# Kernel optimization log

Hardware: AMD Instinct MI355X
Metric: run time of the kernel (lower is better)

## Reference

```python
import jax, jax.numpy as jnp
import numpy as np

N, K = 50000, 16
IN_FEATS, HIDDEN, T2V = 128, 128, 64


def time2vec(t, w0, b0, W, B):
    # t: [..., 1] -> [..., T2V]; linear term + sin periodic terms
    lin = t * w0 + b0                      # [..., 1]
    per = jnp.sin(t * W + B)               # [..., T2V-1]
    return jnp.concatenate([lin, per], axis=-1)


def setup_inputs() -> dict:
    key = jax.random.key(0)
    ks = jax.random.split(key, 12)
    s = 0.05
    return {
        "x": jax.random.normal(ks[0], (N, IN_FEATS), jnp.float32),
        "ts": jax.random.uniform(ks[1], (N, K), jnp.float32),
        "idx": jax.random.randint(ks[2], (N, K), 0, N),
        "t2v_w0": jax.random.normal(ks[3], (1,), jnp.float32),
        "t2v_b0": jax.random.normal(ks[4], (1,), jnp.float32),
        "t2v_W": jax.random.normal(ks[5], (T2V - 1,), jnp.float32),
        "t2v_B": jax.random.normal(ks[6], (T2V - 1,), jnp.float32),
        "Wq": jax.random.normal(ks[7], (IN_FEATS + T2V, HIDDEN), jnp.float32) * s,
        "Wk": jax.random.normal(ks[8], (IN_FEATS + T2V, HIDDEN), jnp.float32) * s,
        "Wv": jax.random.normal(ks[9], (IN_FEATS + T2V, HIDDEN), jnp.float32) * s,
        "Wo": jax.random.normal(ks[10], (HIDDEN, HIDDEN), jnp.float32) * s,
        "bo": jnp.zeros((HIDDEN,), jnp.float32),
    }


def reference(x, ts, idx, t2v_w0, t2v_b0, t2v_W, t2v_B, Wq, Wk, Wv, Wo, bo):
    # Self representation: node feats + time2vec of zero time offset
    te_self = time2vec(jnp.zeros((x.shape[0], 1), x.dtype), t2v_w0, t2v_b0, t2v_W, t2v_B)  # [N, T2V]
    h_self = jnp.concatenate([x, te_self], axis=-1)           # [N, IN+T2V]

    # Neighbor gather + time2vec of interaction times
    x_nbr = x[idx]                                             # [N, K, IN]
    te_nbr = time2vec(ts[..., None], t2v_w0, t2v_b0, t2v_W, t2v_B)  # [N, K, T2V]
    h_nbr = jnp.concatenate([x_nbr, te_nbr], axis=-1)          # [N, K, IN+T2V]

    # Single-head scaled dot-product attention over neighbors
    q = h_self @ Wq                                            # [N, H]
    k = jnp.einsum('nkf,fh->nkh', h_nbr, Wk)                   # [N, K, H]
    v = jnp.einsum('nkf,fh->nkh', h_nbr, Wv)                   # [N, K, H]
    scores = jnp.einsum('nh,nkh->nk', q, k) / jnp.sqrt(jnp.asarray(HIDDEN, x.dtype))
    attn = jax.nn.softmax(scores, axis=-1)                     # [N, K]
    agg = jnp.einsum('nk,nkh->nh', attn, v)                    # [N, H]

    return jax.nn.relu(agg @ Wo + bo)                          # [N, H]
```

## Files before the change

### kernel.cpp

```cpp
#include <hip/hip_runtime.h>
#include <math.h>

#define NN 50000
#define SCL 0.08838834764831845f

#define QC    0
#define CQK   128
#define WT    192
#define BT    256
#define UBASE 320
#define QXB   0
#define KXB   6400000
#define VOB   12800000
#define QKXB  19200000
#define WCAT  22400000
#define WVOP  22457344

typedef __attribute__((ext_vector_type(8))) short bf16x8;
typedef __attribute__((ext_vector_type(4))) float f32x4;

__device__ __forceinline__ float bfl(unsigned int u) {
  union { unsigned int i; float f; } v; v.i = u << 16; return v.f;
}
__device__ __forceinline__ float bfh(unsigned int u) {
  union { unsigned int i; float f; } v; v.i = u & 0xffff0000u; return v.f;
}
__device__ __forceinline__ unsigned short f2bf(float f) {
  union { float f; unsigned int i; } v; v.f = f;
  return (unsigned short)((v.i + 0x7fff + ((v.i >> 16) & 1)) >> 16);
}

__global__ __launch_bounds__(128) void tgat_prep(
    const float* __restrict__ Wq, const float* __restrict__ Wk,
    const float* __restrict__ Wv, const float* __restrict__ Wo,
    const float* __restrict__ t2v_w0, const float* __restrict__ t2v_b0,
    const float* __restrict__ t2v_W, const float* __restrict__ t2v_B,
    float* __restrict__ ws, unsigned short* __restrict__ ub) {
  const int h = threadIdx.x;
  const int b = blockIdx.x;
  __shared__ float row_s[128];

  if (b < 128) {
    const float* wvrow = Wv + b * 128;
    float acc = 0.f;
#pragma unroll 8
    for (int f = 0; f < 128; ++f) acc += wvrow[f] * Wo[f * 128 + h];
    ub[WCAT + (256 + h) * 128 + b] = f2bf(acc);
  } else if (b < 192) {
    const int j = b - 128;
    const float* wvrow = Wv + (128 + j) * 128;
    float acc = 0.f;
#pragma unroll 8
    for (int f = 0; f < 128; ++f) acc += wvrow[f] * Wo[f * 128 + h];
    row_s[h] = acc;
    __syncthreads();
    if (h < 64) {
      unsigned* wp = (unsigned*)(ub + WVOP);
      wp[j * 64 + h] = (unsigned)f2bf(row_s[2 * h]) |
                       ((unsigned)f2bf(row_s[2 * h + 1]) << 16);
    }
  } else if (b == 192) {
    float acc = t2v_b0[0] * Wq[128 * 128 + h];
    for (int j = 1; j < 64; ++j)
      acc += __sinf(t2v_B[j - 1]) * Wq[(128 + j) * 128 + h];
    ws[QC + h] = acc;
  } else if (b < 321) {
    const int f = b - 193;
    if (h < 64) {
      const float* wqrow = Wq + f * 128;
      const float* wkrow = Wk + (128 + h) * 128;
      float acc = 0.f;
#pragma unroll 8
      for (int i = 0; i < 128; ++i) acc += wqrow[i] * wkrow[i];
      ub[WCAT + (384 + h) * 128 + f] = f2bf(SCL * acc);
    }
  } else if (b < 577) {
    const int c = b - 321;
    const float v = (c < 128) ? Wq[h * 128 + c] : Wk[h * 128 + (c - 128)];
    ub[WCAT + c * 128 + h] = f2bf(v);
  } else {
    if (h < 64) {
      ws[WT + h] = (h == 0) ? t2v_w0[0] : t2v_W[h - 1];
      ws[BT + h] = (h == 0) ? t2v_b0[0] : t2v_B[h - 1];
    }
  }
}

__global__ __launch_bounds__(64) void tgat_prep2(
    const float* __restrict__ Wk, float* __restrict__ ws) {
  const int j = threadIdx.x;
  const float* wkrow = Wk + (128 + j) * 128;
  float acc = 0.f;
#pragma unroll 8
  for (int i = 0; i < 128; ++i) acc += ws[QC + i] * wkrow[i];
  ws[CQK + j] = SCL * acc;
}

__global__ __launch_bounds__(256, 4) void tgat_precomp_mfma(
    const float* __restrict__ x, float* ws) {
  const int lane = threadIdx.x & 63;
  const int wv = threadIdx.x >> 6;
  const int mr = blockIdx.x * 128 + wv * 32;
  unsigned short* ub = (unsigned short*)(ws + UBASE);
  const unsigned short* wc = ub + WCAT;
  const int arow = lane & 15;
  const int ko = (lane >> 4) * 8;
  const int rbase = (lane >> 4) * 4;

  bf16x8 afr[2][4];
#pragma unroll
  for (int tile = 0; tile < 2; ++tile) {
    const int row = mr + tile * 16 + arow;
    const float* xrow = x + (size_t)((row < NN) ? row : (NN - 1)) * 128;
#pragma unroll
    for (int kk = 0; kk < 4; ++kk) {
      const float4 lo = *(const float4*)(xrow + kk * 32 + ko);
      const float4 hi = *(const float4*)(xrow + kk * 32 + ko + 4);
      bf16x8 f;
      f[0] = (short)f2bf(lo.x); f[1] = (short)f2bf(lo.y);
      f[2] = (short)f2bf(lo.z); f[3] = (short)f2bf(lo.w);
      f[4] = (short)f2bf(hi.x); f[5] = (short)f2bf(hi.y);
      f[6] = (short)f2bf(hi.z); f[7] = (short)f2bf(hi.w);
      afr[tile][kk] = f;
    }
  }

  unsigned short* qxb  = ub + QXB;
  unsigned short* kxb  = ub + KXB;
  unsigned short* vob  = ub + VOB;
  unsigned short* qkxb = ub + QKXB;

#pragma unroll 2
  for (int ct = 0; ct < 28; ++ct) {
    const int col = ct * 16 + arow;
    bf16x8 bfr[4];
#pragma unroll
    for (int kk = 0; kk < 4; ++kk)
      bfr[kk] = *(const bf16x8*)(wc + (size_t)col * 128 + kk * 32 + ko);
    f32x4 acc0 = {0.f, 0.f, 0.f, 0.f}, acc1 = {0.f, 0.f, 0.f, 0.f};
#pragma unroll
    for (int kk = 0; kk < 4; ++kk) {
      acc0 = __builtin_amdgcn_mfma_f32_16x16x32_bf16(afr[0][kk], bfr[kk], acc0, 0, 0, 0);
      acc1 = __builtin_amdgcn_mfma_f32_16x16x32_bf16(afr[1][kk], bfr[kk], acc1, 0, 0, 0);
    }

    const int gc = ct * 16 + arow;
#pragma unroll
    for (int tile = 0; tile < 2; ++tile) {
      const f32x4 acc = tile ? acc1 : acc0;
      const int r0 = mr + tile * 16 + rbase;
      if (ct < 8) {
        const float qc = ws[QC + gc];
#pragma unroll
        for (int r = 0; r < 4; ++r)
          if (r0 + r < NN)
            qxb[(size_t)(r0 + r) * 128 + gc] = f2bf((acc[r] + qc) * SCL);
      } else if (ct < 16) {
#pragma unroll
        for (int r = 0; r < 4; ++r)
          if (r0 + r < NN)
            kxb[(size_t)(r0 + r) * 128 + (gc - 128)] = f2bf(acc[r]);
      } else if (ct < 24) {
#pragma unroll
        for (int r = 0; r < 4; ++r)
          if (r0 + r < NN)
            vob[(size_t)(r0 + r) * 128 + (gc - 256)] = f2bf(acc[r]);
      } else {
        const float cq = ws[CQK + gc - 384];
#pragma unroll
        for (int r = 0; r < 4; ++r)
          if (r0 + r < NN)
            qkxb[(size_t)(r0 + r) * 64 + (gc - 384)] = f2bf(acc[r] + cq);
      }
    }
  }
}

__global__ __launch_bounds__(256, 4) void tgat_main(
    const float* __restrict__ ts, const int* __restrict__ idx,
    const float* __restrict__ bo, const float* __restrict__ ws,
    float* __restrict__ out) {
  const int lane = threadIdx.x & 63;
  const int wv   = threadIdx.x >> 6;
  const int my_k = lane >> 2, my_c = lane & 3;

  __shared__ float lds[4 * 1312];
  __shared__ unsigned wvo_l[4096];
  float* te_s = lds + wv * 1312;
  float* s_s  = te_s + 1088;
  float* q_s  = te_s + 1104;
  float* qk_s = te_s + 1248;

  const unsigned short* ubr = (const unsigned short*)(ws + UBASE);
  const unsigned short* qxb  = ubr + QXB;
  const unsigned short* kxb  = ubr + KXB;
  const unsigned short* vob  = ubr + VOB;
  const unsigned short* qkxb = ubr + QKXB;

  const int n = blockIdx.x * 4 + wv;

  {
    const uint4* wvp = (const uint4*)(ubr + WVOP);
#pragma unroll
    for (int i = 0; i < 4; ++i)
      ((uint4*)wvo_l)[threadIdx.x + i * 256] = wvp[threadIdx.x + i * 256];
  }

  const int   iv = idx[n * 16 + (lane & 15)];
  const float tv = ts[n * 16 + (lane & 15)];
  const unsigned qu = ((const unsigned*)(qxb + (size_t)n * 128))[lane];
  unsigned qku = 0;
  if (lane < 32) qku = ((const unsigned*)(qkxb + (size_t)n * 64))[lane];
  const float2 bo2 = ((const float2*)bo)[lane];

  const int i_myk = __shfl(iv, my_k, 64);
  const unsigned short* kr = kxb + (size_t)i_myk * 128 + my_c * 32;
  const uint4 kx0 = *(const uint4*)(kr);
  const uint4 kx1 = *(const uint4*)(kr + 8);
  const uint4 kx2 = *(const uint4*)(kr + 16);
  const uint4 kx3 = *(const uint4*)(kr + 24);
  unsigned int vg[16];
#pragma unroll
  for (int k = 0; k < 16; ++k) {
    const int ik = __shfl(iv, k, 64);
    vg[k] = ((const unsigned int*)(vob + (size_t)ik * 128))[lane];
  }

  const float tvk = __shfl(tv, my_k, 64);
  float te[16];
  {
    const float4* w4 = (const float4*)(ws + WT + my_c * 16);
    const float4* b4 = (const float4*)(ws + BT + my_c * 16);
#pragma unroll
    for (int i4 = 0; i4 < 4; ++i4) {
      const float4 a = w4[i4], b = b4[i4];
      te[i4*4+0] = __sinf(tvk * a.x + b.x);
      te[i4*4+1] = __sinf(tvk * a.y + b.y);
      te[i4*4+2] = __sinf(tvk * a.z + b.z);
      te[i4*4+3] = __sinf(tvk * a.w + b.w);
    }
  }
  if (my_c == 0) te[0] = tvk * (ws[WT]) + ws[BT];

  {
    const int f = 2 * lane;
    const int qi = (f >> 5) * 36 + (f & 31);
    q_s[qi] = bfl(qu); q_s[qi + 1] = bfh(qu);
  }
  if (lane < 32) { qk_s[2 * lane] = bfl(qku); qk_s[2 * lane + 1] = bfh(qku); }
#pragma unroll
  for (int i = 0; i < 16; ++i)
    te_s[(my_c * 16 + i) * 17 + my_k] = te[i];
  asm volatile("s_waitcnt lgkmcnt(0)" ::: "memory");

  float p = 0.f;
  {
    const float4* qb = (const float4*)(q_s + my_c * 36);
#pragma unroll
    for (int q8 = 0; q8 < 4; ++q8) {
      const uint4 u = (q8 == 0) ? kx0 : (q8 == 1) ? kx1 : (q8 == 2) ? kx2 : kx3;
      const float4 qlo = qb[q8 * 2], qhi = qb[q8 * 2 + 1];
      p += bfl(u.x) * qlo.x + bfh(u.x) * qlo.y;
      p += bfl(u.y) * qlo.z + bfh(u.y) * qlo.w;
      p += bfl(u.z) * qhi.x + bfh(u.z) * qhi.y;
      p += bfl(u.w) * qhi.z + bfh(u.w) * qhi.w;
    }
    const float4* qq4 = (const float4*)(qk_s + my_c * 16);
#pragma unroll
    for (int i4 = 0; i4 < 4; ++i4) {
      const float4 q = qq4[i4];
      p += te[i4*4+0]*q.x + te[i4*4+1]*q.y + te[i4*4+2]*q.z + te[i4*4+3]*q.w;
    }
  }
  p += __shfl_xor(p, 1, 64);
  p += __shfl_xor(p, 2, 64);
  if (my_c == 0) s_s[my_k] = p;
  asm volatile("s_waitcnt lgkmcnt(0)" ::: "memory");

  float a[16];
  {
    float sv[16];
    const float4* s4 = (const float4*)s_s;
#pragma unroll
    for (int i4 = 0; i4 < 4; ++i4) {
      const float4 v = s4[i4];
      sv[i4*4+0]=v.x; sv[i4*4+1]=v.y; sv[i4*4+2]=v.z; sv[i4*4+3]=v.w;
    }
    float m = sv[0];
#pragma unroll
    for (int k = 1; k < 16; ++k) m = fmaxf(m, sv[k]);
    float sum = 0.f;
#pragma unroll
    for (int k = 0; k < 16; ++k) { a[k] = __expf(sv[k] - m); sum += a[k]; }
    const float inv = 1.f / sum;
#pragma unroll
    for (int k = 0; k < 16; ++k) a[k] *= inv;
  }

  {
    float ta = 0.f;
#pragma unroll
    for (int k = 0; k < 16; ++k) ta += a[k] * te_s[lane * 17 + k];
    qk_s[lane] = ta;
  }
  asm volatile("s_waitcnt lgkmcnt(0)" ::: "memory");

  float acc0 = bo2.x, acc1 = bo2.y;
#pragma unroll
  for (int k = 0; k < 16; ++k) {
    const unsigned int u = vg[k];
    acc0 += a[k] * bfl(u);
    acc1 += a[k] * bfh(u);
  }

  __syncthreads();
  {
    const float4* ta4 = (const float4*)qk_s;
#pragma unroll
    for (int j4 = 0; j4 < 16; ++j4) {
      const float4 tb = ta4[j4];
      const unsigned u0 = wvo_l[(j4*4+0) * 64 + lane];
      const unsigned u1 = wvo_l[(j4*4+1) * 64 + lane];
      const unsigned u2 = wvo_l[(j4*4+2) * 64 + lane];
      const unsigned u3 = wvo_l[(j4*4+3) * 64 + lane];
      acc0 += tb.x * bfl(u0); acc1 += tb.x * bfh(u0);
      acc0 += tb.y * bfl(u1); acc1 += tb.y * bfh(u1);
      acc0 += tb.z * bfl(u2); acc1 += tb.z * bfh(u2);
      acc0 += tb.w * bfl(u3); acc1 += tb.w * bfh(u3);
    }
  }

  float2 o; o.x = fmaxf(acc0, 0.f); o.y = fmaxf(acc1, 0.f);
  ((float2*)(out + (size_t)n * 128))[lane] = o;
}

extern "C" void kernel_launch(void* const* d_in, const int* in_sizes, int n_in,
                              void* d_out, int out_size, void* d_ws, size_t ws_size,
                              hipStream_t stream) {
  const float* x    = (const float*)d_in[0];
  const float* ts   = (const float*)d_in[1];
  const int*   idx  = (const int*)  d_in[2];
  const float* w0   = (const float*)d_in[3];
  const float* b0   = (const float*)d_in[4];
  const float* t2vW = (const float*)d_in[5];
  const float* t2vB = (const float*)d_in[6];
  const float* Wq   = (const float*)d_in[7];
  const float* Wk   = (const float*)d_in[8];
  const float* Wv   = (const float*)d_in[9];
  const float* Wo   = (const float*)d_in[10];
  const float* bo   = (const float*)d_in[11];
  float* ws = (float*)d_ws;
  unsigned short* ub = (unsigned short*)(ws + UBASE);
  float* out = (float*)d_out;

  tgat_prep<<<578, 128, 0, stream>>>(Wq, Wk, Wv, Wo, w0, b0, t2vW, t2vB, ws, ub);
  tgat_prep2<<<1, 64, 0, stream>>>(Wk, ws);
  tgat_precomp_mfma<<<391, 256, 0, stream>>>(x, ws);
  tgat_main<<<12500, 256, 0, stream>>>(ts, idx, bo, ws, out);
}
```

Measured before the change: 226.2 us.

## Split precompute GEMM columns across waves and read Wvo from global instead of LDS

The precompute kernel now gives each block a 16-row tile, with the four waves splitting the 28 column tiles, launched as 3125 blocks instead of 391. This raises parallelism and drops the bounds checks because 50000 divides evenly by 16. The main kernel no longer stages the 16 KB Wvo matrix into shared memory and drops the block barrier. It reads Wvo directly from global/L2 and raises launch bounds to 6 blocks per CU for higher occupancy. The trade-off is more global/L2 loads in the final projection and the x tile being re-read and converted by every wave.

```diff
diff --git a/kernel.cpp b/kernel.cpp
--- a/kernel.cpp
+++ b/kernel.cpp
@@ -96,22 +96,20 @@
   ws[CQK + j] = SCL * acc;
 }
 
-__global__ __launch_bounds__(256, 4) void tgat_precomp_mfma(
+__global__ __launch_bounds__(256) void tgat_precomp_mfma(
     const float* __restrict__ x, float* ws) {
   const int lane = threadIdx.x & 63;
   const int wv = threadIdx.x >> 6;
-  const int mr = blockIdx.x * 128 + wv * 32;
+  const int mr = blockIdx.x * 16;
   unsigned short* ub = (unsigned short*)(ws + UBASE);
   const unsigned short* wc = ub + WCAT;
   const int arow = lane & 15;
   const int ko = (lane >> 4) * 8;
   const int rbase = (lane >> 4) * 4;
 
-  bf16x8 afr[2][4];
-#pragma unroll
-  for (int tile = 0; tile < 2; ++tile) {
-    const int row = mr + tile * 16 + arow;
-    const float* xrow = x + (size_t)((row < NN) ? row : (NN - 1)) * 128;
+  bf16x8 afr[4];
+  {
+    const float* xrow = x + (size_t)(mr + arow) * 128;
 #pragma unroll
     for (int kk = 0; kk < 4; ++kk) {
       const float4 lo = *(const float4*)(xrow + kk * 32 + ko);
@@ -121,7 +119,7 @@
       f[2] = (short)f2bf(lo.z); f[3] = (short)f2bf(lo.w);
       f[4] = (short)f2bf(hi.x); f[5] = (short)f2bf(hi.y);
       f[6] = (short)f2bf(hi.z); f[7] = (short)f2bf(hi.w);
-      afr[tile][kk] = f;
+      afr[kk] = f;
     }
   }
 
@@ -130,53 +128,43 @@
   unsigned short* vob  = ub + VOB;
   unsigned short* qkxb = ub + QKXB;
 
-#pragma unroll 2
-  for (int ct = 0; ct < 28; ++ct) {
+#pragma unroll
+  for (int c7 = 0; c7 < 7; ++c7) {
+    const int ct = wv * 7 + c7;
     const int col = ct * 16 + arow;
     bf16x8 bfr[4];
 #pragma unroll
     for (int kk = 0; kk < 4; ++kk)
       bfr[kk] = *(const bf16x8*)(wc + (size_t)col * 128 + kk * 32 + ko);
-    f32x4 acc0 = {0.f, 0.f, 0.f, 0.f}, acc1 = {0.f, 0.f, 0.f, 0.f};
-#pragma unroll
-    for (int kk = 0; kk < 4; ++kk) {
-      acc0 = __builtin_amdgcn_mfma_f32_16x16x32_bf16(afr[0][kk], bfr[kk], acc0, 0, 0, 0);
-      acc1 = __builtin_amdgcn_mfma_f32_16x16x32_bf16(afr[1][kk], bfr[kk], acc1, 0, 0, 0);
-    }
+    f32x4 acc = {0.f, 0.f, 0.f, 0.f};
+#pragma unroll
+    for (int kk = 0; kk < 4; ++kk)
+      acc = __builtin_amdgcn_mfma_f32_16x16x32_bf16(afr[kk], bfr[kk], acc, 0, 0, 0);
 
     const int gc = ct * 16 + arow;
-#pragma unroll
-    for (int tile = 0; tile < 2; ++tile) {
-      const f32x4 acc = tile ? acc1 : acc0;
-      const int r0 = mr + tile * 16 + rbase;
-      if (ct < 8) {
-        const float qc = ws[QC + gc];
-#pragma unroll
-        for (int r = 0; r < 4; ++r)
-          if (r0 + r < NN)
-            qxb[(size_t)(r0 + r) * 128 + gc] = f2bf((acc[r] + qc) * SCL);
-      } else if (ct < 16) {
-#pragma unroll
-        for (int r = 0; r < 4; ++r)
-          if (r0 + r < NN)
-            kxb[(size_t)(r0 + r) * 128 + (gc - 128)] = f2bf(acc[r]);
-      } else if (ct < 24) {
-#pragma unroll
-        for (int r = 0; r < 4; ++r)
-          if (r0 + r < NN)
-            vob[(size_t)(r0 + r) * 128 + (gc - 256)] = f2bf(acc[r]);
-      } else {
-        const float cq = ws[CQK + gc - 384];
-#pragma unroll
-        for (int r = 0; r < 4; ++r)
-          if (r0 + r < NN)
-            qkxb[(size_t)(r0 + r) * 64 + (gc - 384)] = f2bf(acc[r] + cq);
-      }
-    }
-  }
-}
-
-__global__ __launch_bounds__(256, 4) void tgat_main(
+    if (ct < 8) {
+      const float qc = ws[QC + gc];
+#pragma unroll
+      for (int r = 0; r < 4; ++r)
+        qxb[(size_t)(mr + rbase + r) * 128 + gc] = f2bf((acc[r] + qc) * SCL);
+    } else if (ct < 16) {
+#pragma unroll
+      for (int r = 0; r < 4; ++r)
+        kxb[(size_t)(mr + rbase + r) * 128 + (gc - 128)] = f2bf(acc[r]);
+    } else if (ct < 24) {
+#pragma unroll
+      for (int r = 0; r < 4; ++r)
+        vob[(size_t)(mr + rbase + r) * 128 + (gc - 256)] = f2bf(acc[r]);
+    } else {
+      const float cq = ws[CQK + gc - 384];
+#pragma unroll
+      for (int r = 0; r < 4; ++r)
+        qkxb[(size_t)(mr + rbase + r) * 64 + (gc - 384)] = f2bf(acc[r] + cq);
+    }
+  }
+}
+
+__global__ __launch_bounds__(256, 6) void tgat_main(
     const float* __restrict__ ts, const int* __restrict__ idx,
     const float* __restrict__ bo, const float* __restrict__ ws,
     float* __restrict__ out) {
@@ -185,7 +173,6 @@
   const int my_k = lane >> 2, my_c = lane & 3;
 
   __shared__ float lds[4 * 1312];
-  __shared__ unsigned wvo_l[4096];
   float* te_s = lds + wv * 1312;
   float* s_s  = te_s + 1088;
   float* q_s  = te_s + 1104;
@@ -196,15 +183,9 @@
   const unsigned short* kxb  = ubr + KXB;
   const unsigned short* vob  = ubr + VOB;
   const unsigned short* qkxb = ubr + QKXB;
+  const unsigned* wvp = (const unsigned*)(ubr + WVOP);
 
   const int n = blockIdx.x * 4 + wv;
-
-  {
-    const uint4* wvp = (const uint4*)(ubr + WVOP);
-#pragma unroll
-    for (int i = 0; i < 4; ++i)
-      ((uint4*)wvo_l)[threadIdx.x + i * 256] = wvp[threadIdx.x + i * 256];
-  }
 
   const int   iv = idx[n * 16 + (lane & 15)];
   const float tv = ts[n * 16 + (lane & 15)];
@@ -313,16 +294,15 @@
     acc1 += a[k] * bfh(u);
   }
 
-  __syncthreads();
   {
     const float4* ta4 = (const float4*)qk_s;
 #pragma unroll
     for (int j4 = 0; j4 < 16; ++j4) {
       const float4 tb = ta4[j4];
-      const unsigned u0 = wvo_l[(j4*4+0) * 64 + lane];
-      const unsigned u1 = wvo_l[(j4*4+1) * 64 + lane];
-      const unsigned u2 = wvo_l[(j4*4+2) * 64 + lane];
-      const unsigned u3 = wvo_l[(j4*4+3) * 64 + lane];
+      const unsigned u0 = wvp[(j4*4+0) * 64 + lane];
+      const unsigned u1 = wvp[(j4*4+1) * 64 + lane];
+      const unsigned u2 = wvp[(j4*4+2) * 64 + lane];
+      const unsigned u3 = wvp[(j4*4+3) * 64 + lane];
       acc0 += tb.x * bfl(u0); acc1 += tb.x * bfh(u0);
       acc0 += tb.y * bfl(u1); acc1 += tb.y * bfh(u1);
       acc0 += tb.z * bfl(u2); acc1 += tb.z * bfh(u2);
@@ -355,6 +335,6 @@
 
   tgat_prep<<<578, 128, 0, stream>>>(Wq, Wk, Wv, Wo, w0, b0, t2vW, t2vB, ws, ub);
   tgat_prep2<<<1, 64, 0, stream>>>(Wk, ws);
-  tgat_precomp_mfma<<<391, 256, 0, stream>>>(x, ws);
+  tgat_precomp_mfma<<<3125, 256, 0, stream>>>(x, ws);
   tgat_main<<<12500, 256, 0, stream>>>(ts, idx, bo, ws, out);
 }
```

After: 234.8 us. 1.04x slower.
